# Performance work log

Measured on AMD Instinct MI355X. Metric: run time of the kernel, lower is better.

The kernel has to match this reference:

```python
import jax, jax.numpy as jnp
import numpy as np

B, Q, S, H, D = 4, 1024, 2048, 32, 128  # batch, new tokens, cache capacity, heads, head_dim
SCALE = 0.08838834764831845  # 1/sqrt(128)


def setup_inputs() -> dict:
    key = jax.random.key(0)
    ks = jax.random.split(key, 7)
    query_states = jax.random.normal(ks[0], (B, Q, H, D), jnp.float32)
    key_states = jax.random.normal(ks[1], (B, Q, H, D), jnp.float32)
    value_states = jax.random.normal(ks[2], (B, Q, H, D), jnp.float32)
    k_cache = jax.random.normal(ks[3], (B, S, H, D), jnp.float32)
    v_cache = jax.random.normal(ks[4], (B, S, H, D), jnp.float32)
    q_lens = jax.random.randint(ks[5], (B,), 1, Q + 1).astype(jnp.int32)      # ragged new lengths
    cache_lens = jax.random.randint(ks[6], (B,), 0, Q + 1).astype(jnp.int32)  # prior context lengths
    return dict(query_states=query_states, key_states=key_states, value_states=value_states,
                k_cache=k_cache, v_cache=v_cache, q_lens=q_lens, cache_lens=cache_lens)


def _update_cache(cache, new, cache_lens, q_lens):
    # Per-sequence append: write new[b, :q_len[b]] into cache[b, cache_len[b]:cache_len[b]+q_len[b]]
    def upd(c, n, clen, qlen):
        j = jnp.arange(Q)
        idx = jnp.clip(clen + j, 0, S - 1)               # [Q]
        valid = j < qlen                                  # [Q]
        vals = jnp.where(valid[:, None, None], n, c[idx])  # keep old value where padded
        return c.at[idx].set(vals)
    return jax.vmap(upd)(cache, new, cache_lens, q_lens)


def reference(query_states, key_states, value_states, k_cache, v_cache, q_lens, cache_lens):
    kc = _update_cache(k_cache, key_states, cache_lens, q_lens)   # [B,S,H,D]
    vc = _update_cache(v_cache, value_states, cache_lens, q_lens)

    scores = jnp.einsum('bqhd,bkhd->bhqk', query_states, kc) * SCALE  # [B,H,Q,S]

    qi = jnp.arange(Q)
    kj = jnp.arange(S)
    # query i may attend to cache pos j iff j < cache_len + min(i+1, q_len)  (causal + segment bound)
    limit = cache_lens[:, None] + jnp.minimum(qi[None, :] + 1, q_lens[:, None])  # [B,Q]
    mask = kj[None, None, :] < limit[:, :, None]                                  # [B,Q,S]
    scores = jnp.where(mask[:, None, :, :], scores, -jnp.inf)
    probs = jax.nn.softmax(scores, axis=-1)

    out = jnp.einsum('bhqk,bkhd->bqhd', probs, vc)  # [B,Q,H,D]
    q_valid = (qi[None, :] < q_lens[:, None])[:, :, None, None]
    return jnp.where(q_valid, out, jnp.zeros((), out.dtype))
```

## Files before the change

### kernel.cpp

```cpp
#include <hip/hip_runtime.h>


#define BB 4
#define QQ 1024
#define SS 2048
#define HH 32
#define DD 128
#define QT 64
#define KT 32
#define NTILES 64
#define TILE_ELEMS 4096
#define NITEMS 2048

typedef __attribute__((ext_vector_type(8))) short short8;
typedef __attribute__((ext_vector_type(4))) float f32x4;
typedef __attribute__((ext_vector_type(4))) unsigned int u32x4;
typedef __attribute__((ext_vector_type(8))) unsigned short u16x8;

__device__ __forceinline__ unsigned short f2bf(float f) {
    unsigned int u = __builtin_bit_cast(unsigned int, f);
    u += 0x7FFFu + ((u >> 16) & 1u);
    return (unsigned short)(u >> 16);
}
__device__ __forceinline__ unsigned int pk2(float a, float b) {
    return (unsigned int)f2bf(a) | ((unsigned int)f2bf(b) << 16);
}

__global__ __launch_bounds__(256)
void prep(const float* __restrict__ ks, const float* __restrict__ vs,
          const float* __restrict__ kc, const float* __restrict__ vc,
          const int* __restrict__ qlens, const int* __restrict__ clens,
          unsigned short* __restrict__ Kws, unsigned short* __restrict__ Vws)
{
    const int tile = blockIdx.x, h = blockIdx.y, b = blockIdx.z;
    const int qlen = qlens[b], clen = clens[b];
    if (tile * KT >= clen + qlen) return;
    const int tid = threadIdx.x;
    unsigned short* kout = Kws + (((size_t)b * HH + h) * NTILES + tile) * TILE_ELEMS;
    unsigned short* vout = Vws + (((size_t)b * HH + h) * NTILES + tile) * TILE_ELEMS;

    #pragma unroll
    for (int half = 0; half < 2; ++half) {
        const int key15 = tid & 15, gk = (tid >> 4) & 3, c = tid >> 6;
        int key = tile * KT + half * 16 + key15;
        const float* src;
        if (key < clen) {
            src = kc + (((size_t)b * SS + key) * HH + h) * DD;
        } else {
            int i2 = key - clen; if (i2 > QQ - 1) i2 = QQ - 1;
            src = ks + (((size_t)b * QQ + i2) * HH + h) * DD;
        }
        const int d0 = c * 32 + gk * 8;
        f32x4 a0 = *(const f32x4*)&src[d0];
        f32x4 a1 = *(const f32x4*)&src[d0 + 4];
        u16x8 w;
        w[0] = f2bf(a0[0]); w[1] = f2bf(a0[1]); w[2] = f2bf(a0[2]); w[3] = f2bf(a0[3]);
        w[4] = f2bf(a1[0]); w[5] = f2bf(a1[1]); w[6] = f2bf(a1[2]); w[7] = f2bf(a1[3]);
        *(u16x8*)&kout[half * 2048 + tid * 8] = w;
    }
    #pragma unroll
    for (int it = 0; it < 2; ++it) {
        const int w_ = it * 256 + tid;
        const int lcv = w_ & 15, gv = (w_ >> 4) & 3, n = w_ >> 6;
        const int d = n * 16 + lcv;
        u16x8 w;
        #pragma unroll
        for (int e = 0; e < 8; ++e) {
            int key = tile * KT + gv * 8 + e;
            const float* src;
            if (key < clen) {
                src = vc + (((size_t)b * SS + key) * HH + h) * DD;
            } else {
                int i2 = key - clen; if (i2 > QQ - 1) i2 = QQ - 1;
                src = vs + (((size_t)b * QQ + i2) * HH + h) * DD;
            }
            w[e] = f2bf(src[d]);
        }
        *(u16x8*)&vout[w_ * 8] = w;
    }
}

__global__ __launch_bounds__(256, 4)
void segattn_persist(const float* __restrict__ qs, const int* __restrict__ qlens,
                     const int* __restrict__ clens,
                     const unsigned short* __restrict__ Kws,
                     const unsigned short* __restrict__ Vws,
                     float* __restrict__ out, int* __restrict__ counter)
{
    __shared__ int s_item;
    alignas(16) __shared__ unsigned short KVl[2][8192];

    const int tid = threadIdx.x, wave = tid >> 6, lane = tid & 63;
    const int g = lane >> 4, lc = lane & 15;
    const float psc = 0.08838834764831845f * 1.4426950408889634f;
    const int srcE = ((g & 1) << 1);
    const int addrE = ((srcE << 4) + lc) << 2;
    const int addrO = addrE + 64;
    const bool useB = (g >= 2);
    const int whw = wave * 1024 + lane * 8;

    for (;;) {
        if (tid == 0) s_item = atomicAdd(counter, 1);
        __syncthreads();
        const int idx = s_item;
        __syncthreads();
        if (idx >= NITEMS) break;

        const int qt = 15 - (idx >> 7);
        const int b = idx & 3, h = (idx >> 2) & 31;
        const int qlen = qlens[b], clen = clens[b];
        const int q0 = qt * QT;

        if (q0 >= qlen) {
            f32x4 z = {0.f, 0.f, 0.f, 0.f};
            #pragma unroll
            for (int i2 = 0; i2 < 8; ++i2) {
                int f = tid + i2 * 256;
                int r = f >> 5, d4 = f & 31;
                *(f32x4*)&out[(((size_t)b * QQ + q0 + r) * HH + h) * DD + d4 * 4] = z;
            }
            continue;
        }

        const int q = q0 + wave * 16 + lc;
        const float* qp = qs + (((size_t)b * QQ + q) * HH + h) * DD;
        short8 qf[4];
        #pragma unroll
        for (int c = 0; c < 4; ++c) {
            f32x4 a0 = *(const f32x4*)&qp[c * 32 + g * 8];
            f32x4 a1 = *(const f32x4*)&qp[c * 32 + g * 8 + 4];
            short8 t;
            t[0] = (short)f2bf(a0[0] * psc); t[1] = (short)f2bf(a0[1] * psc);
            t[2] = (short)f2bf(a0[2] * psc); t[3] = (short)f2bf(a0[3] * psc);
            t[4] = (short)f2bf(a1[0] * psc); t[5] = (short)f2bf(a1[1] * psc);
            t[6] = (short)f2bf(a1[2] * psc); t[7] = (short)f2bf(a1[3] * psc);
            qf[c] = t;
        }

        const int lim_l = (q < qlen) ? (clen + q + 1) : 0;
        const int wq0 = q0 + (__builtin_amdgcn_readfirstlane(wave) << 4);
        const int lim_min = (wq0 + 15 < qlen) ? (clen + wq0 + 1) : 0;

        float m_ = -3e38f, l_ = 0.f;
        f32x4 o[8];
        #pragma unroll
        for (int n = 0; n < 8; ++n) o[n] = (f32x4){0.f, 0.f, 0.f, 0.f};

        const int kmax = clen + min(q0 + QT, qlen);
        const int nt = (kmax + KT - 1) / KT;
        const unsigned short* Kb = Kws + ((size_t)(b * HH + h)) * NTILES * TILE_ELEMS;
        const unsigned short* Vb = Vws + ((size_t)(b * HH + h)) * NTILES * TILE_ELEMS;

        {
            u32x4 a0 = *(const u32x4*)&Kb[whw];
            u32x4 a1 = *(const u32x4*)&Kb[whw + 512];
            u32x4 a2 = *(const u32x4*)&Vb[whw];
            u32x4 a3 = *(const u32x4*)&Vb[whw + 512];
            *(u32x4*)&KVl[0][whw]              = a0;
            *(u32x4*)&KVl[0][whw + 512]        = a1;
            *(u32x4*)&KVl[0][4096 + whw]       = a2;
            *(u32x4*)&KVl[0][4096 + whw + 512] = a3;
            asm volatile("s_waitcnt lgkmcnt(0)" ::: "memory");
            __builtin_amdgcn_s_barrier();
            __builtin_amdgcn_sched_barrier(0);
        }
        const int t1 = (nt > 1) ? 1 : 0;
        const unsigned short* kt1 = Kb + (size_t)t1 * TILE_ELEMS;
        const unsigned short* vt1 = Vb + (size_t)t1 * TILE_ELEMS;
        u32x4 sk0 = *(const u32x4*)&kt1[whw];
        u32x4 sk1 = *(const u32x4*)&kt1[whw + 512];
        u32x4 sv0 = *(const u32x4*)&vt1[whw];
        u32x4 sv1 = *(const u32x4*)&vt1[whw + 512];

        int cur = 0;
        for (int t = 0; t < nt; ++t) {
            const int nb = cur ^ 1;
            *(u32x4*)&KVl[nb][whw]              = sk0;
            *(u32x4*)&KVl[nb][whw + 512]        = sk1;
            *(u32x4*)&KVl[nb][4096 + whw]       = sv0;
            *(u32x4*)&KVl[nb][4096 + whw + 512] = sv1;
            const int t2c = (t + 2 < nt) ? t + 2 : (nt - 1);
            const unsigned short* kt2 = Kb + (size_t)t2c * TILE_ELEMS;
            const unsigned short* vt2 = Vb + (size_t)t2c * TILE_ELEMS;
            sk0 = *(const u32x4*)&kt2[whw];
            sk1 = *(const u32x4*)&kt2[whw + 512];
            sv0 = *(const u32x4*)&vt2[whw];
            sv1 = *(const u32x4*)&vt2[whw + 512];
            asm volatile("s_waitcnt lgkmcnt(0)" ::: "memory");
            __builtin_amdgcn_s_barrier();
            __builtin_amdgcn_sched_barrier(0);

            const unsigned short* Kc = &KVl[cur][0];
            const int pbase = t * KT;
            f32x4 s0 = {0.f, 0.f, 0.f, 0.f}, s1 = {0.f, 0.f, 0.f, 0.f};
            #pragma unroll
            for (int c = 0; c < 4; ++c) {
                short8 k0 = *(const short8*)&Kc[c * 512 + lane * 8];
                short8 k1 = *(const short8*)&Kc[2048 + c * 512 + lane * 8];
                s0 = __builtin_amdgcn_mfma_f32_16x16x32_bf16(k0, qf[c], s0, 0, 0, 0);
                s1 = __builtin_amdgcn_mfma_f32_16x16x32_bf16(k1, qf[c], s1, 0, 0, 0);
            }
            if (pbase + KT > lim_min) {
                const int kg0 = pbase + g * 4, kg1 = kg0 + 16;
                #pragma unroll
                for (int r = 0; r < 4; ++r) {
                    if (kg0 + r >= lim_l) s0[r] = -3e38f;
                    if (kg1 + r >= lim_l) s1[r] = -3e38f;
                }
            }
            float pm = fmaxf(fmaxf(fmaxf(s0[0], s0[1]), fmaxf(s0[2], s0[3])),
                             fmaxf(fmaxf(s1[0], s1[1]), fmaxf(s1[2], s1[3])));
            if (__any(pm > m_ + 8.0f)) {
                pm = fmaxf(pm, __shfl_xor(pm, 16));
                pm = fmaxf(pm, __shfl_xor(pm, 32));
                const float mn = fmaxf(m_, pm);
                const float alpha = __builtin_amdgcn_exp2f(m_ - mn);
                m_ = mn;
                l_ *= alpha;
                #pragma unroll
                for (int n = 0; n < 8; ++n) {
                    o[n][0] *= alpha; o[n][1] *= alpha;
                    o[n][2] *= alpha; o[n][3] *= alpha;
                }
            }
            float p[8];
            #pragma unroll
            for (int r = 0; r < 4; ++r) {
                p[r]     = __builtin_amdgcn_exp2f(s0[r] - m_);
                p[4 + r] = __builtin_amdgcn_exp2f(s1[r] - m_);
            }
            l_ += ((p[0] + p[1]) + (p[2] + p[3])) + ((p[4] + p[5]) + (p[6] + p[7]));

            const int A0 = (int)pk2(p[0], p[1]), A1 = (int)pk2(p[2], p[3]);
            const int B0 = (int)pk2(p[4], p[5]), B1 = (int)pk2(p[6], p[7]);
            int dw0a = __builtin_amdgcn_ds_bpermute(addrE, A0);
            int dw0b = __builtin_amdgcn_ds_bpermute(addrE, B0);
            int dw1a = __builtin_amdgcn_ds_bpermute(addrE, A1);
            int dw1b = __builtin_amdgcn_ds_bpermute(addrE, B1);
            int dw2a = __builtin_amdgcn_ds_bpermute(addrO, A0);
            int dw2b = __builtin_amdgcn_ds_bpermute(addrO, B0);
            int dw3a = __builtin_amdgcn_ds_bpermute(addrO, A1);
            int dw3b = __builtin_amdgcn_ds_bpermute(addrO, B1);
            u32x4 pbw;
            pbw[0] = (unsigned int)(useB ? dw0b : dw0a);
            pbw[1] = (unsigned int)(useB ? dw1b : dw1a);
            pbw[2] = (unsigned int)(useB ? dw2b : dw2a);
            pbw[3] = (unsigned int)(useB ? dw3b : dw3a);
            const short8 pb = __builtin_bit_cast(short8, pbw);

            #pragma unroll
            for (int n = 0; n < 8; ++n) {
                short8 vr = *(const short8*)&Kc[4096 + n * 512 + lane * 8];
                o[n] = __builtin_amdgcn_mfma_f32_16x16x32_bf16(vr, pb, o[n], 0, 0, 0);
            }

            asm volatile("s_waitcnt lgkmcnt(0)" ::: "memory");
            __builtin_amdgcn_s_barrier();
            __builtin_amdgcn_sched_barrier(0);
            cur = nb;
        }

        float lt = l_;
        lt += __shfl_xor(lt, 16);
        lt += __shfl_xor(lt, 32);
        const bool val = (q < qlen);
        const float inv = val ? (1.0f / lt) : 0.f;
        float* op = out + (((size_t)b * QQ + q) * HH + h) * DD + g * 4;
        #pragma unroll
        for (int n = 0; n < 8; ++n) {
            f32x4 w;
            w[0] = o[n][0] * inv; w[1] = o[n][1] * inv;
            w[2] = o[n][2] * inv; w[3] = o[n][3] * inv;
            *(f32x4*)&op[n * 16] = w;
        }
    }
}

__global__ __launch_bounds__(256)
void segattn(const float* __restrict__ qs, const float* __restrict__ ks,
             const float* __restrict__ vs, const float* __restrict__ kc,
             const float* __restrict__ vc, const int* __restrict__ qlens,
             const int* __restrict__ clens, float* __restrict__ out)
{
    const int qt = blockIdx.x, h = blockIdx.y, b = blockIdx.z;
    const int tid = threadIdx.x, wave = tid >> 6, lane = tid & 63;
    const int g = lane >> 4, lc = lane & 15;
    const int qlen = qlens[b], clen = clens[b];
    const int q0 = qt * QT;
    if (q0 >= qlen) {
        f32x4 z = {0.f, 0.f, 0.f, 0.f};
        #pragma unroll
        for (int i2 = 0; i2 < 8; ++i2) {
            int f = tid + i2 * 256;
            int r = f >> 5, d4 = f & 31;
            *(f32x4*)&out[(((size_t)b * QQ + q0 + r) * HH + h) * DD + d4 * 4] = z;
        }
        return;
    }
    alignas(16) __shared__ unsigned short Kl[KT * DD];
    alignas(16) __shared__ unsigned short Vl[DD * 40];
    alignas(16) __shared__ unsigned short Pl[4][16][40];
    const float psc = 0.08838834764831845f * 1.4426950408889634f;
    const int qrow = q0 + wave * 16 + lc;
    const float* qp = qs + (((size_t)b * QQ + qrow) * HH + h) * DD;
    short8 qf[4];
    #pragma unroll
    for (int c = 0; c < 4; ++c) {
        f32x4 a0 = *(const f32x4*)&qp[c * 32 + g * 8];
        f32x4 a1 = *(const f32x4*)&qp[c * 32 + g * 8 + 4];
        short8 t;
        t[0] = (short)f2bf(a0[0] * psc); t[1] = (short)f2bf(a0[1] * psc);
        t[2] = (short)f2bf(a0[2] * psc); t[3] = (short)f2bf(a0[3] * psc);
        t[4] = (short)f2bf(a1[0] * psc); t[5] = (short)f2bf(a1[1] * psc);
        t[6] = (short)f2bf(a1[2] * psc); t[7] = (short)f2bf(a1[3] * psc);
        qf[c] = t;
    }
    f32x4 o[8];
    #pragma unroll
    for (int n = 0; n < 8; ++n) o[n] = (f32x4){0.f, 0.f, 0.f, 0.f};
    float m_[4] = {-3e38f, -3e38f, -3e38f, -3e38f};
    float l_[4] = {0.f, 0.f, 0.f, 0.f};
    int lim[4];
    #pragma unroll
    for (int qq = 0; qq < 4; ++qq) {
        int i = q0 + wave * 16 + g * 4 + qq;
        lim[qq] = (i < qlen) ? (clen + i + 1) : 0;
    }
    const int kmax = clen + min(q0 + QT, qlen);
    const int nt = (kmax + KT - 1) / KT;
    for (int t = 0; t < nt; ++t) {
        const int pbase = t * KT;
        __syncthreads();
        #pragma unroll
        for (int it = 0; it < 4; ++it) {
            int f = tid + it * 256;
            int key = f >> 5, d4 = f & 31;
            int p = pbase + key;
            const float *srck, *srcv;
            if (p < clen) {
                size_t off = (((size_t)b * SS + p) * HH + h) * DD + d4 * 4;
                srck = kc + off; srcv = vc + off;
            } else {
                int idx = p - clen; if (idx > QQ - 1) idx = QQ - 1;
                size_t off = (((size_t)b * QQ + idx) * HH + h) * DD + d4 * 4;
                srck = ks + off; srcv = vs + off;
            }
            f32x4 kv = *(const f32x4*)srck;
            f32x4 vv = *(const f32x4*)srcv;
            int ei = (key * DD + d4 * 4) ^ ((key & 7) << 3);
            typedef __attribute__((ext_vector_type(4))) unsigned short u16x4;
            u16x4 kb4 = {f2bf(kv[0]), f2bf(kv[1]), f2bf(kv[2]), f2bf(kv[3])};
            *(u16x4*)&Kl[ei] = kb4;
            int d0 = d4 * 4;
            Vl[(d0 + 0) * 40 + key] = f2bf(vv[0]);
            Vl[(d0 + 1) * 40 + key] = f2bf(vv[1]);
            Vl[(d0 + 2) * 40 + key] = f2bf(vv[2]);
            Vl[(d0 + 3) * 40 + key] = f2bf(vv[3]);
        }
        __syncthreads();
        f32x4 sc0 = {0.f, 0.f, 0.f, 0.f}, sc1 = {0.f, 0.f, 0.f, 0.f};
        #pragma unroll
        for (int c = 0; c < 4; ++c) {
            int i0 = (lc * DD + c * 32 + g * 8) ^ ((lc & 7) << 3);
            int i1 = ((16 + lc) * DD + c * 32 + g * 8) ^ (((16 + lc) & 7) << 3);
            short8 k0 = *(const short8*)&Kl[i0];
            short8 k1 = *(const short8*)&Kl[i1];
            sc0 = __builtin_amdgcn_mfma_f32_16x16x32_bf16(qf[c], k0, sc0, 0, 0, 0);
            sc1 = __builtin_amdgcn_mfma_f32_16x16x32_bf16(qf[c], k1, sc1, 0, 0, 0);
        }
        float pr0[4], pr1[4];
        #pragma unroll
        for (int qq = 0; qq < 4; ++qq) {
            float s0 = sc0[qq], s1 = sc1[qq];
            if (pbase + lc >= lim[qq])      s0 = -3e38f;
            if (pbase + 16 + lc >= lim[qq]) s1 = -3e38f;
            float pm = fmaxf(s0, s1);
            #pragma unroll
            for (int d2 = 1; d2 < 16; d2 <<= 1) pm = fmaxf(pm, __shfl_xor(pm, d2));
            float mn = fmaxf(m_[qq], pm);
            float alpha = exp2f(m_[qq] - mn);
            float p0 = exp2f(s0 - mn), p1 = exp2f(s1 - mn);
            float rs = p0 + p1;
            #pragma unroll
            for (int d2 = 1; d2 < 16; d2 <<= 1) rs += __shfl_xor(rs, d2);
            l_[qq] = l_[qq] * alpha + rs;
            m_[qq] = mn;
            pr0[qq] = p0; pr1[qq] = p1;
            #pragma unroll
            for (int n = 0; n < 8; ++n) o[n][qq] *= alpha;
        }
        #pragma unroll
        for (int qq = 0; qq < 4; ++qq) {
            Pl[wave][g * 4 + qq][lc]      = f2bf(pr0[qq]);
            Pl[wave][g * 4 + qq][16 + lc] = f2bf(pr1[qq]);
        }
        short8 pf = *(const short8*)&Pl[wave][lc][g * 8];
        #pragma unroll
        for (int n = 0; n < 8; ++n) {
            short8 vf = *(const short8*)&Vl[(n * 16 + lc) * 40 + g * 8];
            o[n] = __builtin_amdgcn_mfma_f32_16x16x32_bf16(pf, vf, o[n], 0, 0, 0);
        }
    }
    #pragma unroll
    for (int qq = 0; qq < 4; ++qq) {
        int i = q0 + wave * 16 + g * 4 + qq;
        bool val = (i < qlen);
        float inv = val ? (1.0f / l_[qq]) : 0.f;
        size_t ob = (((size_t)b * QQ + i) * HH + h) * DD + lc;
        #pragma unroll
        for (int n = 0; n < 8; ++n)
            out[ob + (size_t)n * 16] = val ? o[n][qq] * inv : 0.f;
    }
}

extern "C" void kernel_launch(void* const* d_in, const int* in_sizes, int n_in,
                              void* d_out, int out_size, void* d_ws, size_t ws_size,
                              hipStream_t stream) {
    const float* qs = (const float*)d_in[0];
    const float* ks = (const float*)d_in[1];
    const float* vs = (const float*)d_in[2];
    const float* kc = (const float*)d_in[3];
    const float* vc = (const float*)d_in[4];
    const int* ql = (const int*)d_in[5];
    const int* cl = (const int*)d_in[6];
    float* o = (float*)d_out;

    const size_t kv_elems = (size_t)BB * HH * NTILES * TILE_ELEMS;
    const size_t kv_bytes = kv_elems * 2 * sizeof(unsigned short);
    const size_t need = kv_bytes + 128;

    if (ws_size >= need) {
        unsigned short* Kws = (unsigned short*)d_ws;
        unsigned short* Vws = Kws + kv_elems;
        int* counter = (int*)((char*)d_ws + kv_bytes);
        hipMemsetAsync(counter, 0, sizeof(int), stream);
        dim3 pgrid(NTILES, HH, BB), pblk(256, 1, 1);
        hipLaunchKernelGGL(prep, pgrid, pblk, 0, stream, ks, vs, kc, vc, ql, cl, Kws, Vws);
        dim3 grid(1024, 1, 1), blk(256, 1, 1);
        hipLaunchKernelGGL(segattn_persist, grid, blk, 0, stream, qs, ql, cl, Kws, Vws, o, counter);
    } else {
        dim3 grid(QQ / QT, HH, BB), blk(256, 1, 1);
        hipLaunchKernelGGL(segattn, grid, blk, 0, stream, qs, ks, vs, kc, vc, ql, cl, o);
    }
}
```

Before: 177.3 us.

## Process two 64-row query blocks per work item sharing each K/V tile

Each work item now covers 128 query rows instead of 64, with every wave holding two 16-row query fragments (A and B). Each K/V tile staged in LDS therefore feeds twice the MFMA work, halving K/V global and LDS traffic per query. The single global work counter becomes eight counters selected by blockIdx, each serving a subset of (batch, head) pairs, which lowers atomic contention and groups heads for L2 reuse. Dropping the occupancy hint from launch bounds allows more registers for the doubled accumulators, at the cost of fewer resident waves and coarser load balancing.

```diff
diff --git a/kernel.cpp b/kernel.cpp
--- a/kernel.cpp
+++ b/kernel.cpp
@@ -10,7 +10,7 @@
 #define KT 32
 #define NTILES 64
 #define TILE_ELEMS 4096
-#define NITEMS 2048
+#define NPERQ 128
 
 typedef __attribute__((ext_vector_type(8))) short short8;
 typedef __attribute__((ext_vector_type(4))) float f32x4;
@@ -80,7 +80,7 @@
     }
 }
 
-__global__ __launch_bounds__(256, 4)
+__global__ __launch_bounds__(256)
 void segattn_persist(const float* __restrict__ qs, const int* __restrict__ qlens,
                      const int* __restrict__ clens,
                      const unsigned short* __restrict__ Kws,
@@ -98,23 +98,26 @@
     const int addrO = addrE + 64;
     const bool useB = (g >= 2);
     const int whw = wave * 1024 + lane * 8;
+    const int cres = blockIdx.x & 7;
+    int* myctr = counter + cres;
 
     for (;;) {
-        if (tid == 0) s_item = atomicAdd(counter, 1);
+        if (tid == 0) s_item = atomicAdd(myctr, 1);
         __syncthreads();
-        const int idx = s_item;
+        const int pop = s_item;
         __syncthreads();
-        if (idx >= NITEMS) break;
-
-        const int qt = 15 - (idx >> 7);
-        const int b = idx & 3, h = (idx >> 2) & 31;
+        if (pop >= NPERQ) break;
+
+        const int bh = cres + (pop & ~7);
+        const int jt = 7 - (pop & 7);
+        const int b = bh & 3, h = bh >> 2;
         const int qlen = qlens[b], clen = clens[b];
-        const int q0 = qt * QT;
+        const int q0 = jt * 128;
 
         if (q0 >= qlen) {
             f32x4 z = {0.f, 0.f, 0.f, 0.f};
             #pragma unroll
-            for (int i2 = 0; i2 < 8; ++i2) {
+            for (int i2 = 0; i2 < 16; ++i2) {
                 int f = tid + i2 * 256;
                 int r = f >> 5, d4 = f & 31;
                 *(f32x4*)&out[(((size_t)b * QQ + q0 + r) * HH + h) * DD + d4 * 4] = z;
@@ -122,31 +125,44 @@
             continue;
         }
 
-        const int q = q0 + wave * 16 + lc;
-        const float* qp = qs + (((size_t)b * QQ + q) * HH + h) * DD;
-        short8 qf[4];
+        const int qA = q0 + wave * 16 + lc, qB = qA + 64;
+        const float* qpA = qs + (((size_t)b * QQ + qA) * HH + h) * DD;
+        const float* qpB = qs + (((size_t)b * QQ + qB) * HH + h) * DD;
+        short8 qfA[4], qfB[4];
         #pragma unroll
         for (int c = 0; c < 4; ++c) {
-            f32x4 a0 = *(const f32x4*)&qp[c * 32 + g * 8];
-            f32x4 a1 = *(const f32x4*)&qp[c * 32 + g * 8 + 4];
-            short8 t;
-            t[0] = (short)f2bf(a0[0] * psc); t[1] = (short)f2bf(a0[1] * psc);
-            t[2] = (short)f2bf(a0[2] * psc); t[3] = (short)f2bf(a0[3] * psc);
-            t[4] = (short)f2bf(a1[0] * psc); t[5] = (short)f2bf(a1[1] * psc);
-            t[6] = (short)f2bf(a1[2] * psc); t[7] = (short)f2bf(a1[3] * psc);
-            qf[c] = t;
-        }
-
-        const int lim_l = (q < qlen) ? (clen + q + 1) : 0;
-        const int wq0 = q0 + (__builtin_amdgcn_readfirstlane(wave) << 4);
-        const int lim_min = (wq0 + 15 < qlen) ? (clen + wq0 + 1) : 0;
-
-        float m_ = -3e38f, l_ = 0.f;
-        f32x4 o[8];
-        #pragma unroll
-        for (int n = 0; n < 8; ++n) o[n] = (f32x4){0.f, 0.f, 0.f, 0.f};
-
-        const int kmax = clen + min(q0 + QT, qlen);
+            f32x4 a0 = *(const f32x4*)&qpA[c * 32 + g * 8];
+            f32x4 a1 = *(const f32x4*)&qpA[c * 32 + g * 8 + 4];
+            f32x4 b0 = *(const f32x4*)&qpB[c * 32 + g * 8];
+            f32x4 b1 = *(const f32x4*)&qpB[c * 32 + g * 8 + 4];
+            short8 ta, tb;
+            ta[0] = (short)f2bf(a0[0] * psc); ta[1] = (short)f2bf(a0[1] * psc);
+            ta[2] = (short)f2bf(a0[2] * psc); ta[3] = (short)f2bf(a0[3] * psc);
+            ta[4] = (short)f2bf(a1[0] * psc); ta[5] = (short)f2bf(a1[1] * psc);
+            ta[6] = (short)f2bf(a1[2] * psc); ta[7] = (short)f2bf(a1[3] * psc);
+            tb[0] = (short)f2bf(b0[0] * psc); tb[1] = (short)f2bf(b0[1] * psc);
+            tb[2] = (short)f2bf(b0[2] * psc); tb[3] = (short)f2bf(b0[3] * psc);
+            tb[4] = (short)f2bf(b1[0] * psc); tb[5] = (short)f2bf(b1[1] * psc);
+            tb[6] = (short)f2bf(b1[2] * psc); tb[7] = (short)f2bf(b1[3] * psc);
+            qfA[c] = ta; qfB[c] = tb;
+        }
+
+        const int limA = (qA < qlen) ? (clen + qA + 1) : 0;
+        const int limB = (qB < qlen) ? (clen + qB + 1) : 0;
+        const int wq0A = q0 + (__builtin_amdgcn_readfirstlane(wave) << 4);
+        const int wq0B = wq0A + 64;
+        const int lim_minA = (wq0A + 15 < qlen) ? (clen + wq0A + 1) : 0;
+        const int lim_minB = (wq0B + 15 < qlen) ? (clen + wq0B + 1) : 0;
+
+        float mA = -3e38f, lA = 0.f, mB = -3e38f, lB = 0.f;
+        f32x4 oA[8], oB[8];
+        #pragma unroll
+        for (int n = 0; n < 8; ++n) {
+            oA[n] = (f32x4){0.f, 0.f, 0.f, 0.f};
+            oB[n] = (f32x4){0.f, 0.f, 0.f, 0.f};
+        }
+
+        const int kmax = clen + min(q0 + 128, qlen);
         const int nt = (kmax + KT - 1) / KT;
         const unsigned short* Kb = Kws + ((size_t)(b * HH + h)) * NTILES * TILE_ELEMS;
         const unsigned short* Vb = Vws + ((size_t)(b * HH + h)) * NTILES * TILE_ELEMS;
@@ -192,66 +208,114 @@
 
             const unsigned short* Kc = &KVl[cur][0];
             const int pbase = t * KT;
-            f32x4 s0 = {0.f, 0.f, 0.f, 0.f}, s1 = {0.f, 0.f, 0.f, 0.f};
+            f32x4 sA0 = {0.f,0.f,0.f,0.f}, sA1 = {0.f,0.f,0.f,0.f};
+            f32x4 sB0 = {0.f,0.f,0.f,0.f}, sB1 = {0.f,0.f,0.f,0.f};
             #pragma unroll
             for (int c = 0; c < 4; ++c) {
                 short8 k0 = *(const short8*)&Kc[c * 512 + lane * 8];
                 short8 k1 = *(const short8*)&Kc[2048 + c * 512 + lane * 8];
-                s0 = __builtin_amdgcn_mfma_f32_16x16x32_bf16(k0, qf[c], s0, 0, 0, 0);
-                s1 = __builtin_amdgcn_mfma_f32_16x16x32_bf16(k1, qf[c], s1, 0, 0, 0);
-            }
-            if (pbase + KT > lim_min) {
-                const int kg0 = pbase + g * 4, kg1 = kg0 + 16;
+                sA0 = __builtin_amdgcn_mfma_f32_16x16x32_bf16(k0, qfA[c], sA0, 0, 0, 0);
+                sA1 = __builtin_amdgcn_mfma_f32_16x16x32_bf16(k1, qfA[c], sA1, 0, 0, 0);
+                sB0 = __builtin_amdgcn_mfma_f32_16x16x32_bf16(k0, qfB[c], sB0, 0, 0, 0);
+                sB1 = __builtin_amdgcn_mfma_f32_16x16x32_bf16(k1, qfB[c], sB1, 0, 0, 0);
+            }
+            const int kg0 = pbase + g * 4, kg1 = kg0 + 16;
+            if (pbase + KT > lim_minA) {
                 #pragma unroll
                 for (int r = 0; r < 4; ++r) {
-                    if (kg0 + r >= lim_l) s0[r] = -3e38f;
-                    if (kg1 + r >= lim_l) s1[r] = -3e38f;
+                    if (kg0 + r >= limA) sA0[r] = -3e38f;
+                    if (kg1 + r >= limA) sA1[r] = -3e38f;
                 }
             }
-            float pm = fmaxf(fmaxf(fmaxf(s0[0], s0[1]), fmaxf(s0[2], s0[3])),
-                             fmaxf(fmaxf(s1[0], s1[1]), fmaxf(s1[2], s1[3])));
-            if (__any(pm > m_ + 8.0f)) {
-                pm = fmaxf(pm, __shfl_xor(pm, 16));
-                pm = fmaxf(pm, __shfl_xor(pm, 32));
-                const float mn = fmaxf(m_, pm);
-                const float alpha = __builtin_amdgcn_exp2f(m_ - mn);
-                m_ = mn;
-                l_ *= alpha;
+            if (pbase + KT > lim_minB) {
+                #pragma unroll
+                for (int r = 0; r < 4; ++r) {
+                    if (kg0 + r >= limB) sB0[r] = -3e38f;
+                    if (kg1 + r >= limB) sB1[r] = -3e38f;
+                }
+            }
+
+            float pmA = fmaxf(fmaxf(fmaxf(sA0[0], sA0[1]), fmaxf(sA0[2], sA0[3])),
+                              fmaxf(fmaxf(sA1[0], sA1[1]), fmaxf(sA1[2], sA1[3])));
+            if (__any(pmA > mA + 8.0f)) {
+                pmA = fmaxf(pmA, __shfl_xor(pmA, 16));
+                pmA = fmaxf(pmA, __shfl_xor(pmA, 32));
+                const float mn = fmaxf(mA, pmA);
+                const float alpha = __builtin_amdgcn_exp2f(mA - mn);
+                mA = mn; lA *= alpha;
                 #pragma unroll
                 for (int n = 0; n < 8; ++n) {
-                    o[n][0] *= alpha; o[n][1] *= alpha;
-                    o[n][2] *= alpha; o[n][3] *= alpha;
+                    oA[n][0] *= alpha; oA[n][1] *= alpha;
+                    oA[n][2] *= alpha; oA[n][3] *= alpha;
                 }
             }
-            float p[8];
+            float pA[8];
             #pragma unroll
             for (int r = 0; r < 4; ++r) {
-                p[r]     = __builtin_amdgcn_exp2f(s0[r] - m_);
-                p[4 + r] = __builtin_amdgcn_exp2f(s1[r] - m_);
-            }
-            l_ += ((p[0] + p[1]) + (p[2] + p[3])) + ((p[4] + p[5]) + (p[6] + p[7]));
-
-            const int A0 = (int)pk2(p[0], p[1]), A1 = (int)pk2(p[2], p[3]);
-            const int B0 = (int)pk2(p[4], p[5]), B1 = (int)pk2(p[6], p[7]);
-            int dw0a = __builtin_amdgcn_ds_bpermute(addrE, A0);
-            int dw0b = __builtin_amdgcn_ds_bpermute(addrE, B0);
-            int dw1a = __builtin_amdgcn_ds_bpermute(addrE, A1);
-            int dw1b = __builtin_amdgcn_ds_bpermute(addrE, B1);
-            int dw2a = __builtin_amdgcn_ds_bpermute(addrO, A0);
-            int dw2b = __builtin_amdgcn_ds_bpermute(addrO, B0);
-            int dw3a = __builtin_amdgcn_ds_bpermute(addrO, A1);
-            int dw3b = __builtin_amdgcn_ds_bpermute(addrO, B1);
-            u32x4 pbw;
-            pbw[0] = (unsigned int)(useB ? dw0b : dw0a);
-            pbw[1] = (unsigned int)(useB ? dw1b : dw1a);
-            pbw[2] = (unsigned int)(useB ? dw2b : dw2a);
-            pbw[3] = (unsigned int)(useB ? dw3b : dw3a);
-            const short8 pb = __builtin_bit_cast(short8, pbw);
+                pA[r]     = __builtin_amdgcn_exp2f(sA0[r] - mA);
+                pA[4 + r] = __builtin_amdgcn_exp2f(sA1[r] - mA);
+            }
+            lA += ((pA[0]+pA[1])+(pA[2]+pA[3])) + ((pA[4]+pA[5])+(pA[6]+pA[7]));
+
+            float pmB = fmaxf(fmaxf(fmaxf(sB0[0], sB0[1]), fmaxf(sB0[2], sB0[3])),
+                              fmaxf(fmaxf(sB1[0], sB1[1]), fmaxf(sB1[2], sB1[3])));
+            if (__any(pmB > mB + 8.0f)) {
+                pmB = fmaxf(pmB, __shfl_xor(pmB, 16));
+                pmB = fmaxf(pmB, __shfl_xor(pmB, 32));
+                const float mn = fmaxf(mB, pmB);
+                const float alpha = __builtin_amdgcn_exp2f(mB - mn);
+                mB = mn; lB *= alpha;
+                #pragma unroll
+                for (int n = 0; n < 8; ++n) {
+                    oB[n][0] *= alpha; oB[n][1] *= alpha;
+                    oB[n][2] *= alpha; oB[n][3] *= alpha;
+                }
+            }
+            float pB[8];
+            #pragma unroll
+            for (int r = 0; r < 4; ++r) {
+                pB[r]     = __builtin_amdgcn_exp2f(sB0[r] - mB);
+                pB[4 + r] = __builtin_amdgcn_exp2f(sB1[r] - mB);
+            }
+            lB += ((pB[0]+pB[1])+(pB[2]+pB[3])) + ((pB[4]+pB[5])+(pB[6]+pB[7]));
+
+            const int A0 = (int)pk2(pA[0], pA[1]), A1 = (int)pk2(pA[2], pA[3]);
+            const int A2 = (int)pk2(pA[4], pA[5]), A3 = (int)pk2(pA[6], pA[7]);
+            const int B0w = (int)pk2(pB[0], pB[1]), B1w = (int)pk2(pB[2], pB[3]);
+            const int B2w = (int)pk2(pB[4], pB[5]), B3w = (int)pk2(pB[6], pB[7]);
+            int a0e = __builtin_amdgcn_ds_bpermute(addrE, A0);
+            int a2e = __builtin_amdgcn_ds_bpermute(addrE, A2);
+            int a1e = __builtin_amdgcn_ds_bpermute(addrE, A1);
+            int a3e = __builtin_amdgcn_ds_bpermute(addrE, A3);
+            int a0o = __builtin_amdgcn_ds_bpermute(addrO, A0);
+            int a2o = __builtin_amdgcn_ds_bpermute(addrO, A2);
+            int a1o = __builtin_amdgcn_ds_bpermute(addrO, A1);
+            int a3o = __builtin_amdgcn_ds_bpermute(addrO, A3);
+            int b0e = __builtin_amdgcn_ds_bpermute(addrE, B0w);
+            int b2e = __builtin_amdgcn_ds_bpermute(addrE, B2w);
+            int b1e = __builtin_amdgcn_ds_bpermute(addrE, B1w);
+            int b3e = __builtin_amdgcn_ds_bpermute(addrE, B3w);
+            int b0o = __builtin_amdgcn_ds_bpermute(addrO, B0w);
+            int b2o = __builtin_amdgcn_ds_bpermute(addrO, B2w);
+            int b1o = __builtin_amdgcn_ds_bpermute(addrO, B1w);
+            int b3o = __builtin_amdgcn_ds_bpermute(addrO, B3w);
+            u32x4 pwA, pwB;
+            pwA[0] = (unsigned int)(useB ? a2e : a0e);
+            pwA[1] = (unsigned int)(useB ? a3e : a1e);
+            pwA[2] = (unsigned int)(useB ? a2o : a0o);
+            pwA[3] = (unsigned int)(useB ? a3o : a1o);
+            pwB[0] = (unsigned int)(useB ? b2e : b0e);
+            pwB[1] = (unsigned int)(useB ? b3e : b1e);
+            pwB[2] = (unsigned int)(useB ? b2o : b0o);
+            pwB[3] = (unsigned int)(useB ? b3o : b1o);
+            const short8 pbA = __builtin_bit_cast(short8, pwA);
+            const short8 pbB = __builtin_bit_cast(short8, pwB);
 
             #pragma unroll
             for (int n = 0; n < 8; ++n) {
                 short8 vr = *(const short8*)&Kc[4096 + n * 512 + lane * 8];
-                o[n] = __builtin_amdgcn_mfma_f32_16x16x32_bf16(vr, pb, o[n], 0, 0, 0);
+                oA[n] = __builtin_amdgcn_mfma_f32_16x16x32_bf16(vr, pbA, oA[n], 0, 0, 0);
+                oB[n] = __builtin_amdgcn_mfma_f32_16x16x32_bf16(vr, pbB, oB[n], 0, 0, 0);
             }
 
             asm volatile("s_waitcnt lgkmcnt(0)" ::: "memory");
@@ -260,18 +324,26 @@
             cur = nb;
         }
 
-        float lt = l_;
-        lt += __shfl_xor(lt, 16);
-        lt += __shfl_xor(lt, 32);
-        const bool val = (q < qlen);
-        const float inv = val ? (1.0f / lt) : 0.f;
-        float* op = out + (((size_t)b * QQ + q) * HH + h) * DD + g * 4;
+        float ltA = lA;
+        ltA += __shfl_xor(ltA, 16);
+        ltA += __shfl_xor(ltA, 32);
+        float ltB = lB;
+        ltB += __shfl_xor(ltB, 16);
+        ltB += __shfl_xor(ltB, 32);
+        const bool valA = (qA < qlen), valB = (qB < qlen);
+        const float invA = valA ? (1.0f / ltA) : 0.f;
+        const float invB = valB ? (1.0f / ltB) : 0.f;
+        float* opA = out + (((size_t)b * QQ + qA) * HH + h) * DD + g * 4;
+        float* opB = out + (((size_t)b * QQ + qB) * HH + h) * DD + g * 4;
         #pragma unroll
         for (int n = 0; n < 8; ++n) {
-            f32x4 w;
-            w[0] = o[n][0] * inv; w[1] = o[n][1] * inv;
-            w[2] = o[n][2] * inv; w[3] = o[n][3] * inv;
-            *(f32x4*)&op[n * 16] = w;
+            f32x4 wa, wb;
+            wa[0] = oA[n][0] * invA; wa[1] = oA[n][1] * invA;
+            wa[2] = oA[n][2] * invA; wa[3] = oA[n][3] * invA;
+            wb[0] = oB[n][0] * invB; wb[1] = oB[n][1] * invB;
+            wb[2] = oB[n][2] * invB; wb[3] = oB[n][3] * invB;
+            *(f32x4*)&opA[n * 16] = wa;
+            *(f32x4*)&opB[n * 16] = wb;
         }
     }
 }
@@ -433,7 +505,7 @@
         unsigned short* Kws = (unsigned short*)d_ws;
         unsigned short* Vws = Kws + kv_elems;
         int* counter = (int*)((char*)d_ws + kv_bytes);
-        hipMemsetAsync(counter, 0, sizeof(int), stream);
+        hipMemsetAsync(counter, 0, 128, stream);
         dim3 pgrid(NTILES, HH, BB), pblk(256, 1, 1);
         hipLaunchKernelGGL(prep, pgrid, pblk, 0, stream, ks, vs, kc, vc, ql, cl, Kws, Vws);
         dim3 grid(1024, 1, 1), blk(256, 1, 1);
```

Measured after the change: 307.7 us. 1.74x slower.

## Switch attention to 32x32x16 MFMA with two 32-query waves per block

Applied to the files above, without the earlier changes.

Rewrites the persistent attention kernel to use 32x32x16 bf16 MFMA tiles. Each of two waves now owns 32 queries instead of four waves owning 16. The prep kernel's K/V workspace layout is reordered to match the new fragment layout. P is repacked with v_cvt_pk_bf16_f32 and one xor-32 shuffle instead of eight ds_bpermutes. The aim is fewer MFMA issues, fewer permute ops and less reduction overhead per tile. In exchange, each wave uses more accumulator registers and each block has half the waves to hide latency.

```diff
diff --git a/kernel.cpp b/kernel.cpp
--- a/kernel.cpp
+++ b/kernel.cpp
@@ -14,6 +14,7 @@
 
 typedef __attribute__((ext_vector_type(8))) short short8;
 typedef __attribute__((ext_vector_type(4))) float f32x4;
+typedef __attribute__((ext_vector_type(16))) float f32x16;
 typedef __attribute__((ext_vector_type(4))) unsigned int u32x4;
 typedef __attribute__((ext_vector_type(8))) unsigned short u16x8;
 
@@ -22,13 +23,15 @@
     u += 0x7FFFu + ((u >> 16) & 1u);
     return (unsigned short)(u >> 16);
 }
-__device__ __forceinline__ unsigned int pk2(float a, float b) {
-    return (unsigned int)f2bf(a) | ((unsigned int)f2bf(b) << 16);
+__device__ __forceinline__ unsigned int cvtpk(float lo, float hi) {
+    unsigned int r;
+    asm("v_cvt_pk_bf16_f32 %0, %1, %2" : "=v"(r) : "v"(lo), "v"(hi));
+    return r;
 }
 
 __global__ __launch_bounds__(256)
 void prep(const float* __restrict__ ks, const float* __restrict__ vs,
-          const float* __restrict__ kc, const float* __restrict__ vc,
+          const float* __restrict__ kc_, const float* __restrict__ vc,
           const int* __restrict__ qlens, const int* __restrict__ clens,
           unsigned short* __restrict__ Kws, unsigned short* __restrict__ Vws)
 {
@@ -40,33 +43,36 @@
     unsigned short* vout = Vws + (((size_t)b * HH + h) * NTILES + tile) * TILE_ELEMS;
 
     #pragma unroll
-    for (int half = 0; half < 2; ++half) {
-        const int key15 = tid & 15, gk = (tid >> 4) & 3, c = tid >> 6;
-        int key = tile * KT + half * 16 + key15;
+    for (int h2 = 0; h2 < 2; ++h2) {
+        const int idx8 = h2 * 2048 + tid * 8;
+        const int c = idx8 >> 9, l = (idx8 >> 3) & 63;
+        int key = tile * KT + (l & 31);
         const float* src;
         if (key < clen) {
-            src = kc + (((size_t)b * SS + key) * HH + h) * DD;
+            src = kc_ + (((size_t)b * SS + key) * HH + h) * DD;
         } else {
             int i2 = key - clen; if (i2 > QQ - 1) i2 = QQ - 1;
             src = ks + (((size_t)b * QQ + i2) * HH + h) * DD;
         }
-        const int d0 = c * 32 + gk * 8;
+        const int d0 = c * 16 + ((l >> 5) << 3);
         f32x4 a0 = *(const f32x4*)&src[d0];
         f32x4 a1 = *(const f32x4*)&src[d0 + 4];
         u16x8 w;
         w[0] = f2bf(a0[0]); w[1] = f2bf(a0[1]); w[2] = f2bf(a0[2]); w[3] = f2bf(a0[3]);
         w[4] = f2bf(a1[0]); w[5] = f2bf(a1[1]); w[6] = f2bf(a1[2]); w[7] = f2bf(a1[3]);
-        *(u16x8*)&kout[half * 2048 + tid * 8] = w;
-    }
-    #pragma unroll
-    for (int it = 0; it < 2; ++it) {
-        const int w_ = it * 256 + tid;
-        const int lcv = w_ & 15, gv = (w_ >> 4) & 3, n = w_ >> 6;
-        const int d = n * 16 + lcv;
+        *(u16x8*)&kout[idx8] = w;
+    }
+    #pragma unroll
+    for (int h2 = 0; h2 < 2; ++h2) {
+        const int idx8 = h2 * 2048 + tid * 8;
+        const int a = idx8 >> 9, l = (idx8 >> 3) & 63;
+        const int dchunk = a >> 1, kcc = a & 1;
+        const int d = dchunk * 32 + (l & 31);
+        const int kb = tile * KT + kcc * 16 + ((l >> 5) << 3);
         u16x8 w;
         #pragma unroll
         for (int e = 0; e < 8; ++e) {
-            int key = tile * KT + gv * 8 + e;
+            int key = kb + e;
             const float* src;
             if (key < clen) {
                 src = vc + (((size_t)b * SS + key) * HH + h) * DD;
@@ -76,11 +82,11 @@
             }
             w[e] = f2bf(src[d]);
         }
-        *(u16x8*)&vout[w_ * 8] = w;
-    }
-}
-
-__global__ __launch_bounds__(256, 4)
+        *(u16x8*)&vout[idx8] = w;
+    }
+}
+
+__global__ __launch_bounds__(128, 2)
 void segattn_persist(const float* __restrict__ qs, const int* __restrict__ qlens,
                      const int* __restrict__ clens,
                      const unsigned short* __restrict__ Kws,
@@ -90,14 +96,11 @@
     __shared__ int s_item;
     alignas(16) __shared__ unsigned short KVl[2][8192];
 
-    const int tid = threadIdx.x, wave = tid >> 6, lane = tid & 63;
-    const int g = lane >> 4, lc = lane & 15;
+    const int tid = threadIdx.x, w = tid >> 6, lane = tid & 63;
+    const int q31 = lane & 31, hi = lane >> 5;
+    const bool hiL = (hi != 0);
     const float psc = 0.08838834764831845f * 1.4426950408889634f;
-    const int srcE = ((g & 1) << 1);
-    const int addrE = ((srcE << 4) + lc) << 2;
-    const int addrO = addrE + 64;
-    const bool useB = (g >= 2);
-    const int whw = wave * 1024 + lane * 8;
+    const int sbase = w * 2048 + lane * 8;
 
     for (;;) {
         if (tid == 0) s_item = atomicAdd(counter, 1);
@@ -114,21 +117,22 @@
         if (q0 >= qlen) {
             f32x4 z = {0.f, 0.f, 0.f, 0.f};
             #pragma unroll
-            for (int i2 = 0; i2 < 8; ++i2) {
-                int f = tid + i2 * 256;
+            for (int i2 = 0; i2 < 16; ++i2) {
+                int f = tid + i2 * 128;
                 int r = f >> 5, d4 = f & 31;
                 *(f32x4*)&out[(((size_t)b * QQ + q0 + r) * HH + h) * DD + d4 * 4] = z;
             }
             continue;
         }
 
-        const int q = q0 + wave * 16 + lc;
+        const int q = q0 + w * 32 + q31;
         const float* qp = qs + (((size_t)b * QQ + q) * HH + h) * DD;
-        short8 qf[4];
-        #pragma unroll
-        for (int c = 0; c < 4; ++c) {
-            f32x4 a0 = *(const f32x4*)&qp[c * 32 + g * 8];
-            f32x4 a1 = *(const f32x4*)&qp[c * 32 + g * 8 + 4];
+        short8 qf[8];
+        #pragma unroll
+        for (int c = 0; c < 8; ++c) {
+            const int d0 = c * 16 + hi * 8;
+            f32x4 a0 = *(const f32x4*)&qp[d0];
+            f32x4 a1 = *(const f32x4*)&qp[d0 + 4];
             short8 t;
             t[0] = (short)f2bf(a0[0] * psc); t[1] = (short)f2bf(a0[1] * psc);
             t[2] = (short)f2bf(a0[2] * psc); t[3] = (short)f2bf(a0[3] * psc);
@@ -138,13 +142,11 @@
         }
 
         const int lim_l = (q < qlen) ? (clen + q + 1) : 0;
-        const int wq0 = q0 + (__builtin_amdgcn_readfirstlane(wave) << 4);
-        const int lim_min = (wq0 + 15 < qlen) ? (clen + wq0 + 1) : 0;
+        const int wq0 = q0 + w * 32;
+        const int lim_min = (wq0 + 31 < qlen) ? (clen + wq0 + 1) : 0;
 
         float m_ = -3e38f, l_ = 0.f;
-        f32x4 o[8];
-        #pragma unroll
-        for (int n = 0; n < 8; ++n) o[n] = (f32x4){0.f, 0.f, 0.f, 0.f};
+        f32x16 o0 = {0}, o1 = {0}, o2 = {0}, o3 = {0};
 
         const int kmax = clen + min(q0 + QT, qlen);
         const int nt = (kmax + KT - 1) / KT;
@@ -152,14 +154,13 @@
         const unsigned short* Vb = Vws + ((size_t)(b * HH + h)) * NTILES * TILE_ELEMS;
 
         {
-            u32x4 a0 = *(const u32x4*)&Kb[whw];
-            u32x4 a1 = *(const u32x4*)&Kb[whw + 512];
-            u32x4 a2 = *(const u32x4*)&Vb[whw];
-            u32x4 a3 = *(const u32x4*)&Vb[whw + 512];
-            *(u32x4*)&KVl[0][whw]              = a0;
-            *(u32x4*)&KVl[0][whw + 512]        = a1;
-            *(u32x4*)&KVl[0][4096 + whw]       = a2;
-            *(u32x4*)&KVl[0][4096 + whw + 512] = a3;
+            #pragma unroll
+            for (int j = 0; j < 4; ++j) {
+                u32x4 ak = *(const u32x4*)&Kb[sbase + j * 512];
+                u32x4 av = *(const u32x4*)&Vb[sbase + j * 512];
+                *(u32x4*)&KVl[0][sbase + j * 512]        = ak;
+                *(u32x4*)&KVl[0][4096 + sbase + j * 512] = av;
+            }
             asm volatile("s_waitcnt lgkmcnt(0)" ::: "memory");
             __builtin_amdgcn_s_barrier();
             __builtin_amdgcn_sched_barrier(0);
@@ -167,91 +168,124 @@
         const int t1 = (nt > 1) ? 1 : 0;
         const unsigned short* kt1 = Kb + (size_t)t1 * TILE_ELEMS;
         const unsigned short* vt1 = Vb + (size_t)t1 * TILE_ELEMS;
-        u32x4 sk0 = *(const u32x4*)&kt1[whw];
-        u32x4 sk1 = *(const u32x4*)&kt1[whw + 512];
-        u32x4 sv0 = *(const u32x4*)&vt1[whw];
-        u32x4 sv1 = *(const u32x4*)&vt1[whw + 512];
+        u32x4 sk0 = *(const u32x4*)&kt1[sbase];
+        u32x4 sk1 = *(const u32x4*)&kt1[sbase + 512];
+        u32x4 sk2 = *(const u32x4*)&kt1[sbase + 1024];
+        u32x4 sk3 = *(const u32x4*)&kt1[sbase + 1536];
+        u32x4 sv0 = *(const u32x4*)&vt1[sbase];
+        u32x4 sv1 = *(const u32x4*)&vt1[sbase + 512];
+        u32x4 sv2 = *(const u32x4*)&vt1[sbase + 1024];
+        u32x4 sv3 = *(const u32x4*)&vt1[sbase + 1536];
 
         int cur = 0;
         for (int t = 0; t < nt; ++t) {
             const int nb = cur ^ 1;
-            *(u32x4*)&KVl[nb][whw]              = sk0;
-            *(u32x4*)&KVl[nb][whw + 512]        = sk1;
-            *(u32x4*)&KVl[nb][4096 + whw]       = sv0;
-            *(u32x4*)&KVl[nb][4096 + whw + 512] = sv1;
+            *(u32x4*)&KVl[nb][sbase]               = sk0;
+            *(u32x4*)&KVl[nb][sbase + 512]         = sk1;
+            *(u32x4*)&KVl[nb][sbase + 1024]        = sk2;
+            *(u32x4*)&KVl[nb][sbase + 1536]        = sk3;
+            *(u32x4*)&KVl[nb][4096 + sbase]        = sv0;
+            *(u32x4*)&KVl[nb][4096 + sbase + 512]  = sv1;
+            *(u32x4*)&KVl[nb][4096 + sbase + 1024] = sv2;
+            *(u32x4*)&KVl[nb][4096 + sbase + 1536] = sv3;
             const int t2c = (t + 2 < nt) ? t + 2 : (nt - 1);
             const unsigned short* kt2 = Kb + (size_t)t2c * TILE_ELEMS;
             const unsigned short* vt2 = Vb + (size_t)t2c * TILE_ELEMS;
-            sk0 = *(const u32x4*)&kt2[whw];
-            sk1 = *(const u32x4*)&kt2[whw + 512];
-            sv0 = *(const u32x4*)&vt2[whw];
-            sv1 = *(const u32x4*)&vt2[whw + 512];
+            sk0 = *(const u32x4*)&kt2[sbase];
+            sk1 = *(const u32x4*)&kt2[sbase + 512];
+            sk2 = *(const u32x4*)&kt2[sbase + 1024];
+            sk3 = *(const u32x4*)&kt2[sbase + 1536];
+            sv0 = *(const u32x4*)&vt2[sbase];
+            sv1 = *(const u32x4*)&vt2[sbase + 512];
+            sv2 = *(const u32x4*)&vt2[sbase + 1024];
+            sv3 = *(const u32x4*)&vt2[sbase + 1536];
             asm volatile("s_waitcnt lgkmcnt(0)" ::: "memory");
             __builtin_amdgcn_s_barrier();
             __builtin_amdgcn_sched_barrier(0);
 
             const unsigned short* Kc = &KVl[cur][0];
             const int pbase = t * KT;
-            f32x4 s0 = {0.f, 0.f, 0.f, 0.f}, s1 = {0.f, 0.f, 0.f, 0.f};
-            #pragma unroll
-            for (int c = 0; c < 4; ++c) {
-                short8 k0 = *(const short8*)&Kc[c * 512 + lane * 8];
-                short8 k1 = *(const short8*)&Kc[2048 + c * 512 + lane * 8];
-                s0 = __builtin_amdgcn_mfma_f32_16x16x32_bf16(k0, qf[c], s0, 0, 0, 0);
-                s1 = __builtin_amdgcn_mfma_f32_16x16x32_bf16(k1, qf[c], s1, 0, 0, 0);
+            f32x16 s = {0};
+            #pragma unroll
+            for (int c = 0; c < 8; ++c) {
+                short8 kf = *(const short8*)&Kc[c * 512 + lane * 8];
+                s = __builtin_amdgcn_mfma_f32_32x32x16_bf16(kf, qf[c], s, 0, 0, 0);
             }
             if (pbase + KT > lim_min) {
-                const int kg0 = pbase + g * 4, kg1 = kg0 + 16;
                 #pragma unroll
-                for (int r = 0; r < 4; ++r) {
-                    if (kg0 + r >= lim_l) s0[r] = -3e38f;
-                    if (kg1 + r >= lim_l) s1[r] = -3e38f;
+                for (int r = 0; r < 16; ++r) {
+                    const int kk = pbase + (r & 3) + ((r >> 2) << 3) + hi * 4;
+                    if (kk >= lim_l) s[r] = -3e38f;
                 }
             }
-            float pm = fmaxf(fmaxf(fmaxf(s0[0], s0[1]), fmaxf(s0[2], s0[3])),
-                             fmaxf(fmaxf(s1[0], s1[1]), fmaxf(s1[2], s1[3])));
+            float pm = fmaxf(fmaxf(fmaxf(fmaxf(s[0], s[1]), fmaxf(s[2], s[3])),
+                                   fmaxf(fmaxf(s[4], s[5]), fmaxf(s[6], s[7]))),
+                             fmaxf(fmaxf(fmaxf(s[8], s[9]), fmaxf(s[10], s[11])),
+                                   fmaxf(fmaxf(s[12], s[13]), fmaxf(s[14], s[15]))));
             if (__any(pm > m_ + 8.0f)) {
-                pm = fmaxf(pm, __shfl_xor(pm, 16));
                 pm = fmaxf(pm, __shfl_xor(pm, 32));
                 const float mn = fmaxf(m_, pm);
                 const float alpha = __builtin_amdgcn_exp2f(m_ - mn);
                 m_ = mn;
                 l_ *= alpha;
                 #pragma unroll
-                for (int n = 0; n < 8; ++n) {
-                    o[n][0] *= alpha; o[n][1] *= alpha;
-                    o[n][2] *= alpha; o[n][3] *= alpha;
+                for (int r = 0; r < 16; ++r) {
+                    o0[r] *= alpha; o1[r] *= alpha; o2[r] *= alpha; o3[r] *= alpha;
                 }
             }
-            float p[8];
-            #pragma unroll
-            for (int r = 0; r < 4; ++r) {
-                p[r]     = __builtin_amdgcn_exp2f(s0[r] - m_);
-                p[4 + r] = __builtin_amdgcn_exp2f(s1[r] - m_);
-            }
-            l_ += ((p[0] + p[1]) + (p[2] + p[3])) + ((p[4] + p[5]) + (p[6] + p[7]));
-
-            const int A0 = (int)pk2(p[0], p[1]), A1 = (int)pk2(p[2], p[3]);
-            const int B0 = (int)pk2(p[4], p[5]), B1 = (int)pk2(p[6], p[7]);
-            int dw0a = __builtin_amdgcn_ds_bpermute(addrE, A0);
-            int dw0b = __builtin_amdgcn_ds_bpermute(addrE, B0);
-            int dw1a = __builtin_amdgcn_ds_bpermute(addrE, A1);
-            int dw1b = __builtin_amdgcn_ds_bpermute(addrE, B1);
-            int dw2a = __builtin_amdgcn_ds_bpermute(addrO, A0);
-            int dw2b = __builtin_amdgcn_ds_bpermute(addrO, B0);
-            int dw3a = __builtin_amdgcn_ds_bpermute(addrO, A1);
-            int dw3b = __builtin_amdgcn_ds_bpermute(addrO, B1);
-            u32x4 pbw;
-            pbw[0] = (unsigned int)(useB ? dw0b : dw0a);
-            pbw[1] = (unsigned int)(useB ? dw1b : dw1a);
-            pbw[2] = (unsigned int)(useB ? dw2b : dw2a);
-            pbw[3] = (unsigned int)(useB ? dw3b : dw3a);
-            const short8 pb = __builtin_bit_cast(short8, pbw);
-
-            #pragma unroll
-            for (int n = 0; n < 8; ++n) {
-                short8 vr = *(const short8*)&Kc[4096 + n * 512 + lane * 8];
-                o[n] = __builtin_amdgcn_mfma_f32_16x16x32_bf16(vr, pb, o[n], 0, 0, 0);
+            float p[16];
+            #pragma unroll
+            for (int r = 0; r < 16; ++r) p[r] = __builtin_amdgcn_exp2f(s[r] - m_);
+            l_ += (((p[0]+p[1])+(p[2]+p[3])) + ((p[4]+p[5])+(p[6]+p[7])))
+                + (((p[8]+p[9])+(p[10]+p[11])) + ((p[12]+p[13])+(p[14]+p[15])));
+
+            const unsigned int w0 = cvtpk(p[0],  p[1]);
+            const unsigned int w1 = cvtpk(p[2],  p[3]);
+            const unsigned int w2 = cvtpk(p[4],  p[5]);
+            const unsigned int w3 = cvtpk(p[6],  p[7]);
+            const unsigned int w4 = cvtpk(p[8],  p[9]);
+            const unsigned int w5 = cvtpk(p[10], p[11]);
+            const unsigned int w6 = cvtpk(p[12], p[13]);
+            const unsigned int w7 = cvtpk(p[14], p[15]);
+            const unsigned int x0 = (unsigned int)__shfl_xor((int)w0, 32);
+            const unsigned int x1 = (unsigned int)__shfl_xor((int)w1, 32);
+            const unsigned int x2 = (unsigned int)__shfl_xor((int)w2, 32);
+            const unsigned int x3 = (unsigned int)__shfl_xor((int)w3, 32);
+            const unsigned int x4 = (unsigned int)__shfl_xor((int)w4, 32);
+            const unsigned int x5 = (unsigned int)__shfl_xor((int)w5, 32);
+            const unsigned int x6 = (unsigned int)__shfl_xor((int)w6, 32);
+            const unsigned int x7 = (unsigned int)__shfl_xor((int)w7, 32);
+            u32x4 pb0w, pb1w;
+            pb0w[0] = hiL ? x2 : w0;  pb0w[1] = hiL ? x3 : w1;
+            pb0w[2] = hiL ? w2 : x0;  pb0w[3] = hiL ? w3 : x1;
+            pb1w[0] = hiL ? x6 : w4;  pb1w[1] = hiL ? x7 : w5;
+            pb1w[2] = hiL ? w6 : x4;  pb1w[3] = hiL ? w7 : x5;
+            const short8 pb0 = __builtin_bit_cast(short8, pb0w);
+            const short8 pb1 = __builtin_bit_cast(short8, pb1w);
+
+            {
+                short8 va = *(const short8*)&Kc[4096 + 0 * 512 + lane * 8];
+                short8 vb = *(const short8*)&Kc[4096 + 1 * 512 + lane * 8];
+                o0 = __builtin_amdgcn_mfma_f32_32x32x16_bf16(va, pb0, o0, 0, 0, 0);
+                o0 = __builtin_amdgcn_mfma_f32_32x32x16_bf16(vb, pb1, o0, 0, 0, 0);
+            }
+            {
+                short8 va = *(const short8*)&Kc[4096 + 2 * 512 + lane * 8];
+                short8 vb = *(const short8*)&Kc[4096 + 3 * 512 + lane * 8];
+                o1 = __builtin_amdgcn_mfma_f32_32x32x16_bf16(va, pb0, o1, 0, 0, 0);
+                o1 = __builtin_amdgcn_mfma_f32_32x32x16_bf16(vb, pb1, o1, 0, 0, 0);
+            }
+            {
+                short8 va = *(const short8*)&Kc[4096 + 4 * 512 + lane * 8];
+                short8 vb = *(const short8*)&Kc[4096 + 5 * 512 + lane * 8];
+                o2 = __builtin_amdgcn_mfma_f32_32x32x16_bf16(va, pb0, o2, 0, 0, 0);
+                o2 = __builtin_amdgcn_mfma_f32_32x32x16_bf16(vb, pb1, o2, 0, 0, 0);
+            }
+            {
+                short8 va = *(const short8*)&Kc[4096 + 6 * 512 + lane * 8];
+                short8 vb = *(const short8*)&Kc[4096 + 7 * 512 + lane * 8];
+                o3 = __builtin_amdgcn_mfma_f32_32x32x16_bf16(va, pb0, o3, 0, 0, 0);
+                o3 = __builtin_amdgcn_mfma_f32_32x32x16_bf16(vb, pb1, o3, 0, 0, 0);
             }
 
             asm volatile("s_waitcnt lgkmcnt(0)" ::: "memory");
@@ -260,18 +294,26 @@
             cur = nb;
         }
 
-        float lt = l_;
-        lt += __shfl_xor(lt, 16);
-        lt += __shfl_xor(lt, 32);
+        float lt = l_ + __shfl_xor(l_, 32);
         const bool val = (q < qlen);
         const float inv = val ? (1.0f / lt) : 0.f;
-        float* op = out + (((size_t)b * QQ + q) * HH + h) * DD + g * 4;
-        #pragma unroll
-        for (int n = 0; n < 8; ++n) {
-            f32x4 w;
-            w[0] = o[n][0] * inv; w[1] = o[n][1] * inv;
-            w[2] = o[n][2] * inv; w[3] = o[n][3] * inv;
-            *(f32x4*)&op[n * 16] = w;
+        float* op = out + (((size_t)b * QQ + q) * HH + h) * DD;
+        #pragma unroll
+        for (int rr = 0; rr < 4; ++rr) {
+            f32x4 wv;
+            const int d0 = rr * 8 + hi * 4;
+            wv[0] = o0[rr*4+0]*inv; wv[1] = o0[rr*4+1]*inv;
+            wv[2] = o0[rr*4+2]*inv; wv[3] = o0[rr*4+3]*inv;
+            *(f32x4*)&op[d0] = wv;
+            wv[0] = o1[rr*4+0]*inv; wv[1] = o1[rr*4+1]*inv;
+            wv[2] = o1[rr*4+2]*inv; wv[3] = o1[rr*4+3]*inv;
+            *(f32x4*)&op[32 + d0] = wv;
+            wv[0] = o2[rr*4+0]*inv; wv[1] = o2[rr*4+1]*inv;
+            wv[2] = o2[rr*4+2]*inv; wv[3] = o2[rr*4+3]*inv;
+            *(f32x4*)&op[64 + d0] = wv;
+            wv[0] = o3[rr*4+0]*inv; wv[1] = o3[rr*4+1]*inv;
+            wv[2] = o3[rr*4+2]*inv; wv[3] = o3[rr*4+3]*inv;
+            *(f32x4*)&op[96 + d0] = wv;
         }
     }
 }
@@ -436,7 +478,7 @@
         hipMemsetAsync(counter, 0, sizeof(int), stream);
         dim3 pgrid(NTILES, HH, BB), pblk(256, 1, 1);
         hipLaunchKernelGGL(prep, pgrid, pblk, 0, stream, ks, vs, kc, vc, ql, cl, Kws, Vws);
-        dim3 grid(1024, 1, 1), blk(256, 1, 1);
+        dim3 grid(1024, 1, 1), blk(128, 1, 1);
         hipLaunchKernelGGL(segattn_persist, grid, blk, 0, stream, qs, ql, cl, Kws, Vws, o, counter);
     } else {
         dim3 grid(QQ / QT, HH, BB), blk(256, 1, 1);
```

Result: faster. 169.6 us (-4.4%).
